# Optimization experiments

Hardware: AMD Instinct MI355X
Metric: run time of the kernel (lower is better)

The kernel has to match this reference:

```python
import jax, jax.numpy as jnp
import numpy as np

H = 768; R = 16; L = 3; NS = 128; NQ = 128


def setup_inputs():
    key = jax.random.key(0)
    ks = iter(jax.random.split(key, 40))
    def w(shape, s=0.02):
        return (s * jax.random.normal(next(ks), shape)).astype(jnp.float32)
    return {
        "support_features": jax.random.normal(next(ks), (NS, H), jnp.float32),
        "support_labels": jax.random.randint(next(ks), (NS,), 0, 3),
        "query_features": jax.random.normal(next(ks), (NQ, H), jnp.float32),
        "sim_w1": w((H, 2 * H)), "sim_b1": jnp.zeros((H,), jnp.float32),
        "sim_w2": w((R, H)), "sim_b2": jnp.zeros((R,), jnp.float32),
        "div_w1": w((H, 2 * H)), "div_b1": jnp.zeros((H,), jnp.float32),
        "div_w2": w((R, H)), "div_b2": jnp.zeros((R,), jnp.float32),
        "rel_w": w((L, R, H, H)), "rel_b": jnp.zeros((L, R, H), jnp.float32),
        "agg_w1": w((L, H, 2 * H)), "agg_b1": jnp.zeros((L, H), jnp.float32),
        "agg_w2": w((L, H, H)), "agg_b2": jnp.zeros((L, H), jnp.float32),
        "ln_g": jnp.ones((L, H), jnp.float32), "ln_b": jnp.zeros((L, H), jnp.float32),
        "cls_w1": w((H // 2, H)), "cls_b1": jnp.zeros((H // 2,), jnp.float32),
        "cls_w2": w((3, H // 2)), "cls_b2": jnp.zeros((3,), jnp.float32),
    }


def _symmetrize(F):
    # torch loop fills [i,j] and [j,i] with value computed from pair (min(i,j), max(i,j)); diag stays 0
    N = F.shape[0]
    idx = jnp.arange(N)
    lower = (idx[:, None] > idx[None, :])
    Fs = jnp.where(lower[:, :, None], jnp.swapaxes(F, 0, 1), F)
    off = (idx[:, None] != idx[None, :]).astype(F.dtype)
    return Fs * off[:, :, None]


def _relations(x, w1, b1, w2, b2, diversity):
    h = x.shape[1]
    wa, wb = w1[:, :h], w1[:, h:]  # split concat([a,b]) @ w1^T into two matmuls
    pa = x @ wa.T                  # [N,H], contribution of first element (x_i)
    if diversity:
        d = jnp.abs(x[:, None, :] - x[None, :, :])   # [N,N,H]
        hid = jax.nn.relu(pa[:, None, :] + d @ wb.T + b1)
    else:
        pb = x @ wb.T
        hid = jax.nn.relu(pa[:, None, :] + pb[None, :, :] + b1)
    logits = hid @ w2.T + b2       # [N,N,R]
    return _symmetrize(jax.nn.softmax(logits, axis=-1))


def _layer_norm(y, g, b):
    mu = y.mean(-1, keepdims=True)
    var = ((y - mu) ** 2).mean(-1, keepdims=True)
    return (y - mu) / jnp.sqrt(var + 1e-5) * g + b


def _prop_layer(x, C, rw, rb, aw1, ab1, aw2, ab2, g, b):
    N = x.shape[0]
    T = jnp.einsum('jh,rkh->jrk', x, rw) + rb       # per-relation transform [N,R,H]
    msg = jnp.einsum('ijr,jrk->ik', C, T) / (N - 1)  # mean over N-1 neighbors (diag of C is 0)
    comb = jnp.concatenate([x, msg], axis=-1)
    agg = jax.nn.relu(comb @ aw1.T + ab1) @ aw2.T + ab2
    return _layer_norm(agg + x, g, b)


def reference(support_features, support_labels, query_features,
              sim_w1, sim_b1, sim_w2, sim_b2,
              div_w1, div_b1, div_w2, div_b2,
              rel_w, rel_b, agg_w1, agg_b1, agg_w2, agg_b2, ln_g, ln_b,
              cls_w1, cls_b1, cls_w2, cls_b2):
    all_x = jnp.concatenate([support_features, query_features], axis=0)
    sim = _relations(all_x, sim_w1, sim_b1, sim_w2, sim_b2, diversity=False)
    div = _relations(all_x, div_w1, div_b1, div_w2, div_b2, diversity=True)
    C = (sim + div) * 0.5
    x = all_x
    for l in range(L):
        x = _prop_layer(x, C, rel_w[l], rel_b[l], agg_w1[l], agg_b1[l],
                        agg_w2[l], agg_b2[l], ln_g[l], ln_b[l])
    q = x[support_features.shape[0]:]
    preds = jax.nn.relu(q @ cls_w1.T + cls_b1) @ cls_w2.T + cls_b2  # dropout = identity (eval)
    return preds, sim, div, x
```

## Files before the change

kernel.cpp:

```cpp
#include <hip/hip_runtime.h>
#include <hip/hip_bf16.h>
#include <hip/hip_fp16.h>


typedef __attribute__((ext_vector_type(8))) short s16x8;
typedef __attribute__((ext_vector_type(4))) float f32x4;

__device__ __forceinline__ short f2bf_s(float f){
  union { __hip_bfloat16 h; short s; } u; u.h = __float2bfloat16(f); return u.s;
}
__device__ __forceinline__ float bf_s2f(short s){
  union { __hip_bfloat16 h; short s; } u; u.s = s; return __bfloat162float(u.h);
}
__device__ __forceinline__ short f2h_s(float f){
  union { __half h; short s; } u; u.h = __float2half(f); return u.s;
}
__device__ __forceinline__ f32x4 mfma16(s16x8 a, s16x8 b, f32x4 c){
  return __builtin_amdgcn_mfma_f32_16x16x32_bf16(a, b, c, 0, 0, 0);
}
__device__ __forceinline__ f32x4 mfma16h(s16x8 a, s16x8 b, f32x4 c){
  return __builtin_amdgcn_mfma_f32_16x16x32_f16(a, b, c, 0, 0, 0);
}
__device__ __forceinline__ void gload16(void* lds, const void* g){
  __builtin_amdgcn_global_load_lds((const __attribute__((address_space(1))) void*)g,
                                   (__attribute__((address_space(3))) void*)lds,
                                   16, 0, 0);
}
__device__ __forceinline__ unsigned pack2bf(float lo, float hi){
  return __builtin_amdgcn_perm(__float_as_uint(hi), __float_as_uint(lo), 0x07060302u);
}
__device__ __forceinline__ s16x8 absdiff_h(uint4 a, uint4 b){
  union { s16x8 v; unsigned u[4]; } o;
  const unsigned au[4] = {a.x,a.y,a.z,a.w}, bu[4] = {b.x,b.y,b.z,b.w};
  #pragma unroll
  for (int w = 0; w < 4; ++w){
    unsigned d;
    asm("v_pk_add_f16 %0, %1, %2 neg_lo:[0,1] neg_hi:[0,1]"
        : "=v"(d) : "v"(au[w]), "v"(bu[w]));
    o.u[w] = d & 0x7fff7fffu;
  }
  return o.v;
}

__device__ __forceinline__ void tri_decode32(int b, int& i0, int& j0){
  int jb = (int)((sqrtf((float)b + 1.f) - 1.f)*0.5f);
  while (4*(jb+1)*(jb+2) <= b) ++jb;
  while (4*jb*(jb+1) > b) --jb;
  i0 = (b - 4*jb*(jb+1))*4;
  j0 = jb*32;
}

template<int BM, int BN, int EPI>
__global__ __launch_bounds__(256) void gemm_bt2(
    const short* __restrict__ A, int lda,
    const short* __restrict__ B, int ldb,
    float* __restrict__ Cf, short* __restrict__ Cb, int ldc,
    const float* __restrict__ bias, int K, int NT)
{
  __shared__ short As[BM*128];
  __shared__ short Bs[BN*128];
  const int tid = threadIdx.x, lane = tid & 63, wid = tid >> 6;
  const int nt = blockIdx.x % NT, mt = blockIdx.x / NT;
  const int m0 = mt*BM, n0 = nt*BN;
  const int wm0 = (wid>>1)*(BM/2), wn0 = (wid&1)*(BN/2);
  f32x4 acc[BM/32][BN/32] = {};
  for (int k0 = 0; k0 < K; k0 += 128){
    if (k0) __syncthreads();
    #pragma unroll
    for (int q = 0; q < BM/16; ++q){
      const int d = (wid*(BM/16)+q)*1024 + lane*16;
      const int row = d>>8, c = d&255;
      gload16((char*)As + (wid*(BM/16)+q)*1024,
              (const char*)A + (size_t)(m0+row)*lda*2 + (size_t)k0*2 + (c ^ ((row&7)<<4)));
    }
    #pragma unroll
    for (int q = 0; q < BN/16; ++q){
      const int d = (wid*(BN/16)+q)*1024 + lane*16;
      const int row = d>>8, c = d&255;
      gload16((char*)Bs + (wid*(BN/16)+q)*1024,
              (const char*)B + (size_t)(n0+row)*ldb*2 + (size_t)k0*2 + (c ^ ((row&7)<<4)));
    }
    __syncthreads();
    #pragma unroll
    for (int kk = 0; kk < 4; ++kk){
      const int colb = (kk*32 + (lane>>4)*8)*2;
      s16x8 af[BM/32], bfv[BN/32];
      #pragma unroll
      for (int mi = 0; mi < BM/32; ++mi){
        const int row = wm0 + mi*16 + (lane&15);
        af[mi] = *(const s16x8*)((char*)As + row*256 + (colb ^ ((row&7)<<4)));
      }
      #pragma unroll
      for (int ni = 0; ni < BN/32; ++ni){
        const int row = wn0 + ni*16 + (lane&15);
        bfv[ni] = *(const s16x8*)((char*)Bs + row*256 + (colb ^ ((row&7)<<4)));
      }
      #pragma unroll
      for (int mi = 0; mi < BM/32; ++mi)
        #pragma unroll
        for (int ni = 0; ni < BN/32; ++ni)
          acc[mi][ni] = mfma16(af[mi], bfv[ni], acc[mi][ni]);
    }
  }
  #pragma unroll
  for (int mi = 0; mi < BM/32; ++mi){
    #pragma unroll
    for (int ni = 0; ni < BN/32; ++ni){
      const int gcol = n0 + wn0 + ni*16 + (lane&15);
      const float bv = bias[gcol];
      #pragma unroll
      for (int r = 0; r < 4; ++r){
        const int grow = m0 + wm0 + mi*16 + (lane>>4)*4 + r;
        float v = acc[mi][ni][r] + bv;
        if (EPI == 2) v = fmaxf(v, 0.f);
        if (EPI == 3) Cf[(size_t)grow*ldc + gcol] = v;
        else          Cb[(size_t)grow*ldc + gcol] = f2bf_s(v);
      }
    }
  }
}

__global__ __launch_bounds__(256) void gemm_msg(
    const short* __restrict__ A,
    const short* __restrict__ B,
    float* __restrict__ slabs)
{
  __shared__ short As[64*64];
  __shared__ short Bs[64*64];
  const int tid = threadIdx.x, lane = tid & 63, wid = tid >> 6;
  const int mt = blockIdx.x / 12, nt = blockIdx.x % 12;
  const int m0 = mt*64, n0 = nt*64, kc0 = blockIdx.y*512;
  const int wm0 = (wid>>1)*32, wn0 = (wid&1)*32;
  f32x4 acc[2][2] = {};
  for (int s = 0; s < 8; ++s){
    const int k0 = kc0 + s*64;
    if (s) __syncthreads();
    #pragma unroll
    for (int q = 0; q < 2; ++q){
      const int d = (wid*2+q)*1024 + lane*16;
      const int row = d>>7, c = d&127;
      gload16((char*)As + (wid*2+q)*1024,
              (const char*)A + (size_t)(m0+row)*8192 + (size_t)k0*2 + (c ^ ((row&7)<<4)));
    }
    #pragma unroll
    for (int rd = 0; rd < 2; ++rd){
      int ei = rd*2048 + tid*8, kr = ei>>6, nc = ei&63;
      union { uint4 v; short s4[8]; } u;
      u.v = *(const uint4*)(B + (size_t)(k0+kr)*768 + n0 + nc);
      #pragma unroll
      for (int e = 0; e < 8; ++e)
        *(short*)((char*)Bs + (nc+e)*128 + ((kr*2) ^ (((nc+e)&7)<<4))) = u.s4[e];
    }
    __syncthreads();
    #pragma unroll
    for (int kk = 0; kk < 2; ++kk){
      const int colb = (kk*32 + (lane>>4)*8)*2;
      s16x8 af[2], bfv[2];
      #pragma unroll
      for (int mi = 0; mi < 2; ++mi){
        const int row = wm0 + mi*16 + (lane&15);
        af[mi] = *(const s16x8*)((char*)As + row*128 + (colb ^ ((row&7)<<4)));
      }
      #pragma unroll
      for (int ni = 0; ni < 2; ++ni){
        const int row = wn0 + ni*16 + (lane&15);
        bfv[ni] = *(const s16x8*)((char*)Bs + row*128 + (colb ^ ((row&7)<<4)));
      }
      #pragma unroll
      for (int mi = 0; mi < 2; ++mi)
        #pragma unroll
        for (int ni = 0; ni < 2; ++ni)
          acc[mi][ni] = mfma16(af[mi], bfv[ni], acc[mi][ni]);
    }
  }
  float* out = slabs + (size_t)blockIdx.y*196608;
  #pragma unroll
  for (int mi = 0; mi < 2; ++mi)
    #pragma unroll
    for (int ni = 0; ni < 2; ++ni){
      const int gcol = n0 + wn0 + ni*16 + (lane&15);
      #pragma unroll
      for (int r = 0; r < 4; ++r){
        const int grow = m0 + wm0 + mi*16 + (lane>>4)*4 + r;
        out[(size_t)grow*768 + gcol] = acc[mi][ni][r];
      }
    }
}

__global__ void msgsum(const float* __restrict__ slabs, short* __restrict__ comb){
  const int i = (blockIdx.x*256 + threadIdx.x)*4;
  if (i >= 196608) return;
  float4 s = {0.f,0.f,0.f,0.f};
  #pragma unroll
  for (int c = 0; c < 8; ++c){
    float4 v = *(const float4*)(slabs + (size_t)c*196608 + i);
    s.x += v.x; s.y += v.y; s.z += v.z; s.w += v.w;
  }
  const float sc = 1.f/255.f;
  const int row = i/768, col = i%768;
  union { uint2 u; short s4[4]; } o;
  o.s4[0]=f2bf_s(s.x*sc); o.s4[1]=f2bf_s(s.y*sc);
  o.s4[2]=f2bf_s(s.z*sc); o.s4[3]=f2bf_s(s.w*sc);
  *(uint2*)(comb + (size_t)row*1536 + 768 + col) = o.u;
}

__global__ __launch_bounds__(512, 4) void pairrel5(
    const short* __restrict__ xh,
    const short* __restrict__ wbdh,
    const float* __restrict__ P2,
    const short* __restrict__ w2d_g,
    const short* __restrict__ w2s_g,
    float* __restrict__ Ldp,
    float* __restrict__ Ls)
{
  __shared__ short Bs[2*256*64];
  const int tid = threadIdx.x, lane = tid & 63, wv = tid >> 6;
  int i0, j0; tri_decode32(blockIdx.x, i0, j0);

  if (blockIdx.y == 3){
    f32x4 acc2 = {0.f,0.f,0.f,0.f};
    const int arow = wv*16 + (lane&15);
    for (int nt = 0; nt < 3; ++nt){
      const int n0 = nt*256;
      if (nt) __syncthreads();
      {
        const int row = tid>>2, c0 = (tid&3)*64;
        const float* pap = P2 + (size_t)(i0 + (row>>5))*2304 + n0 + c0;
        const float* pbp = P2 + (size_t)(j0 + (row&31))*2304 + 768 + n0 + c0;
        #pragma unroll
        for (int cc = 0; cc < 64; cc += 8){
          float4 a0 = *(const float4*)(pap+cc), a1 = *(const float4*)(pap+cc+4);
          float4 q0 = *(const float4*)(pbp+cc), q1 = *(const float4*)(pbp+cc+4);
          uint4 o;
          o.x = pack2bf(fmaxf(a0.x+q0.x,0.f), fmaxf(a0.y+q0.y,0.f));
          o.y = pack2bf(fmaxf(a0.z+q0.z,0.f), fmaxf(a0.w+q0.w,0.f));
          o.z = pack2bf(fmaxf(a1.x+q1.x,0.f), fmaxf(a1.y+q1.y,0.f));
          o.w = pack2bf(fmaxf(a1.z+q1.z,0.f), fmaxf(a1.w+q1.w,0.f));
          *(uint4*)((char*)Bs + row*512 + (((c0+cc)*2) ^ ((row&7)<<4))) = o;
        }
      }
      __syncthreads();
      #pragma unroll
      for (int q = 0; q < 8; ++q){
        const int colb = (q*32 + (lane>>4)*8)*2;
        s16x8 a = *(const s16x8*)((const char*)Bs + arow*512 + (colb ^ ((arow&7)<<4)));
        s16x8 w = *(const s16x8*)(w2s_g + (size_t)(lane&15)*768 + n0 + q*32 + (lane>>4)*8);
        acc2 = mfma16(a, w, acc2);
      }
    }
    const int r_ = lane & 15;
    #pragma unroll
    for (int r = 0; r < 4; ++r){
      const int p = wv*16 + (lane>>4)*4 + r;
      const int i = i0 + (p>>5), j = j0 + (p&31);
      Ls[(((size_t)i<<8) + j)*16 + r_] = acc2[r];
    }
    return;
  }

  const int ip = wv >> 2, jj = (wv >> 1) & 1, wc = wv & 1;
  const int nt = blockIdx.y, n0 = nt*256;

  const short* xjp  = xh + (size_t)(j0 + jj*16 + (lane&15))*768 + (lane>>4)*8;
  const short* xi0p = xh + (size_t)(i0 + 2*ip    )*768 + (lane>>4)*8;
  const short* xi1p = xh + (size_t)(i0 + 2*ip + 1)*768 + (lane>>4)*8;

  #pragma unroll
  for (int q = 0; q < 4; ++q){
    const int d = (wv*4+q)*1024 + lane*16;
    const int row = d>>7, c = d&127;
    gload16((char*)Bs + (wv*4+q)*1024,
            (const char*)wbdh + (size_t)(n0+row)*1536 + (c ^ ((row&7)<<4)));
  }

  f32x4 acc[2][8] = {};
  for (int t = 0; t < 12; ++t){
    uint4 uja  = *(const uint4*)(xjp  + t*64);
    uint4 ujb  = *(const uint4*)(xjp  + t*64 + 32);
    uint4 ui0a = *(const uint4*)(xi0p + t*64);
    uint4 ui0b = *(const uint4*)(xi0p + t*64 + 32);
    uint4 ui1a = *(const uint4*)(xi1p + t*64);
    uint4 ui1b = *(const uint4*)(xi1p + t*64 + 32);
    if (t < 11){
      char* dst = (char*)Bs + ((t+1)&1)*32768;
      const char* src = (const char*)wbdh + (size_t)(t+1)*128;
      #pragma unroll
      for (int q = 0; q < 4; ++q){
        const int d = (wv*4+q)*1024 + lane*16;
        const int row = d>>7, c = d&127;
        gload16(dst + (wv*4+q)*1024, src + (size_t)(n0+row)*1536 + (c ^ ((row&7)<<4)));
      }
    }
    __builtin_amdgcn_sched_barrier(0);
    if (t < 11) asm volatile("s_waitcnt vmcnt(10)" ::: "memory");
    else        asm volatile("s_waitcnt vmcnt(6)"  ::: "memory");
    __builtin_amdgcn_s_barrier();
    __builtin_amdgcn_sched_barrier(0);
    const char* bufc = (const char*)Bs + (t&1)*32768;
    #pragma unroll
    for (int kk = 0; kk < 2; ++kk){
      s16x8 af0 = absdiff_h(kk ? ujb : uja, kk ? ui0b : ui0a);
      s16x8 af1 = absdiff_h(kk ? ujb : uja, kk ? ui1b : ui1a);
      const int colb = (kk*32 + (lane>>4)*8)*2;
      #pragma unroll
      for (int ni = 0; ni < 8; ++ni){
        const int row = wc*128 + ni*16 + (lane&15);
        s16x8 bv = *(const s16x8*)(bufc + row*128 + (colb ^ ((row&7)<<4)));
        acc[0][ni] = mfma16h(af0, bv, acc[0][ni]);
        acc[1][ni] = mfma16h(af1, bv, acc[1][ni]);
      }
    }
    __builtin_amdgcn_sched_barrier(0);
    __builtin_amdgcn_s_barrier();
  }
  __syncthreads();

  float* red = (float*)((char*)Bs + 32768);
  #pragma unroll
  for (int h = 0; h < 2; ++h){
    if (ip == h){
      #pragma unroll
      for (int mi = 0; mi < 2; ++mi){
        const float* pr = P2 + (size_t)(i0 + 2*h + mi)*2304 + 1536 + n0;
        #pragma unroll
        for (int ni = 0; ni < 8; ++ni){
          const int col = wc*128 + ni*16 + (lane&15);
          const float pav = pr[col];
          #pragma unroll
          for (int r = 0; r < 4; ++r){
            const int lrow = mi*32 + jj*16 + (lane>>4)*4 + r;
            const float v = fmaxf(acc[mi][ni][r] + pav, 0.f);
            *(short*)((char*)Bs + lrow*512 + ((col*2) ^ ((lrow&7)<<4))) =
                (short)(__float_as_uint(v) >> 16);
          }
        }
      }
    }
    __syncthreads();
    const int kh = wv >> 2, rq = wv & 3;
    f32x4 a2 = {0.f,0.f,0.f,0.f};
    const int arow = rq*16 + (lane&15);
    #pragma unroll
    for (int q = 0; q < 4; ++q){
      const int k = kh*128 + q*32 + (lane>>4)*8;
      s16x8 a = *(const s16x8*)((char*)Bs + arow*512 + ((k*2) ^ ((arow&7)<<4)));
      s16x8 w = *(const s16x8*)(w2d_g + (size_t)(lane&15)*768 + n0 + k);
      a2 = mfma16(a, w, a2);
    }
    if (kh == 1){
      #pragma unroll
      for (int r = 0; r < 4; ++r)
        red[(rq*16 + (lane>>4)*4 + r)*16 + (lane&15)] = a2[r];
    }
    __syncthreads();
    if (kh == 0){
      #pragma unroll
      for (int r = 0; r < 4; ++r){
        const int lrow = rq*16 + (lane>>4)*4 + r;
        const int p = h*64 + lrow;
        const int i = i0 + (p>>5), j = j0 + (p&31);
        Ldp[(size_t)nt*1048576 + (((size_t)i<<8) + j)*16 + (lane&15)]
          = a2[r] + red[lrow*16 + (lane&15)];
      }
    }
    __syncthreads();
  }
}

__global__ __launch_bounds__(256) void finisher2(
    const float* __restrict__ Ls, const float* __restrict__ Ldp,
    const float* __restrict__ b2s, const float* __restrict__ b2d,
    float* __restrict__ simo, float* __restrict__ divo, short* __restrict__ Cb)
{
  const int p = blockIdx.x*256 + threadIdx.x;
  const int i = p >> 8, j = p & 255;
  float so[16], dd[16];
  if (i == j){
    #pragma unroll
    for (int r = 0; r < 16; ++r){ so[r] = 0.f; dd[r] = 0.f; }
  } else {
    const int si = i < j ? i : j, sj = i < j ? j : i;
    const size_t base = (((size_t)si << 8) + sj) * 16;
    float mx = -1e30f, sum;
    #pragma unroll
    for (int r = 0; r < 16; ++r){ so[r] = Ls[base+r] + b2s[r]; mx = fmaxf(mx, so[r]); }
    sum = 0.f;
    #pragma unroll
    for (int r = 0; r < 16; ++r){ so[r] = expf(so[r]-mx); sum += so[r]; }
    sum = 1.f/sum;
    #pragma unroll
    for (int r = 0; r < 16; ++r) so[r] *= sum;
    mx = -1e30f;
    #pragma unroll
    for (int r = 0; r < 16; ++r){
      dd[r] = Ldp[base+r] + Ldp[base+r+1048576] + Ldp[base+r+2097152] + b2d[r];
      mx = fmaxf(mx, dd[r]);
    }
    sum = 0.f;
    #pragma unroll
    for (int r = 0; r < 16; ++r){ dd[r] = expf(dd[r]-mx); sum += dd[r]; }
    sum = 1.f/sum;
    #pragma unroll
    for (int r = 0; r < 16; ++r) dd[r] *= sum;
  }
  const size_t ob = (size_t)p * 16;
  #pragma unroll
  for (int r = 0; r < 16; ++r){
    simo[ob+r] = so[r];
    divo[ob+r] = dd[r];
    Cb[ob+r]   = f2bf_s(0.5f*(so[r]+dd[r]));
  }
}

__global__ __launch_bounds__(256) void gemm_relT(
    const short* __restrict__ A,
    const float* __restrict__ Bf,
    short* __restrict__ T,
    const float* __restrict__ bias)
{
  __shared__ short As[128*64];
  __shared__ short Bs[64*64];
  const int tid = threadIdx.x, lane = tid & 63, wv = tid >> 6;
  const int nt = blockIdx.x >> 1, mt = blockIdx.x & 1;
  const int n0 = nt*64, m0 = mt*128;
  const int wm = wv >> 1, wn = wv & 1;
  const int brow = tid >> 2, q4 = tid & 3;
  f32x4 acc[4][2] = {};
  for (int k0 = 0; k0 < 768; k0 += 64){
    if (k0) __syncthreads();
    #pragma unroll
    for (int q = 0; q < 4; ++q){
      const int d = (wv*4+q)*1024 + lane*16;
      const int row = d>>7, c = d&127;
      gload16((char*)As + (wv*4+q)*1024,
              (const char*)A + (size_t)(m0+row)*3072 + (size_t)k0*2 + (c ^ ((row&7)<<4)));
    }
    {
      const float* bp = Bf + (size_t)(n0+brow)*768 + k0 + q4*16;
      float4 v0 = *(const float4*)bp,      v1 = *(const float4*)(bp+4);
      float4 v2 = *(const float4*)(bp+8),  v3 = *(const float4*)(bp+12);
      union { uint4 v; unsigned u[4]; } ua, ub;
      ua.u[0]=pack2bf(v0.x,v0.y); ua.u[1]=pack2bf(v0.z,v0.w);
      ua.u[2]=pack2bf(v1.x,v1.y); ua.u[3]=pack2bf(v1.z,v1.w);
      ub.u[0]=pack2bf(v2.x,v2.y); ub.u[1]=pack2bf(v2.z,v2.w);
      ub.u[2]=pack2bf(v3.x,v3.y); ub.u[3]=pack2bf(v3.z,v3.w);
      const int bc = q4*32;
      *(uint4*)((char*)Bs + brow*128 + ((bc   ) ^ ((brow&7)<<4))) = ua.v;
      *(uint4*)((char*)Bs + brow*128 + ((bc+16) ^ ((brow&7)<<4))) = ub.v;
    }
    __syncthreads();
    #pragma unroll
    for (int kk = 0; kk < 2; ++kk){
      const int kb = kk*64 + (lane>>4)*16;
      s16x8 af[4], bfv[2];
      #pragma unroll
      for (int mi = 0; mi < 4; ++mi){
        const int row = wm*64 + mi*16 + (lane&15);
        af[mi] = *(const s16x8*)((char*)As + row*128 + (kb ^ ((row&7)<<4)));
      }
      #pragma unroll
      for (int ni = 0; ni < 2; ++ni){
        const int row = wn*32 + ni*16 + (lane&15);
        bfv[ni] = *(const s16x8*)((char*)Bs + row*128 + (kb ^ ((row&7)<<4)));
      }
      #pragma unroll
      for (int mi = 0; mi < 4; ++mi)
        #pragma unroll
        for (int ni = 0; ni < 2; ++ni)
          acc[mi][ni] = mfma16(af[mi], bfv[ni], acc[mi][ni]);
    }
  }
  #pragma unroll
  for (int mi = 0; mi < 4; ++mi)
    #pragma unroll
    for (int ni = 0; ni < 2; ++ni){
      const int nn = n0 + wn*32 + ni*16 + (lane&15);
      const float bv = bias[nn];
      #pragma unroll
      for (int r = 0; r < 4; ++r){
        const int row = m0 + wm*64 + mi*16 + (lane>>4)*4 + r;
        T[(size_t)row*12288 + nn] = f2bf_s(acc[mi][ni][r] + bv);
      }
    }
}

__global__ __launch_bounds__(256) void ln_kernel(
    const float* __restrict__ y, float* __restrict__ x, short* __restrict__ combx,
    const float* __restrict__ g, const float* __restrict__ b, float* __restrict__ xfinal)
{
  const int row = blockIdx.x, tid = threadIdx.x;
  float tv[3]; float s = 0.f, s2 = 0.f;
  #pragma unroll
  for (int c = 0; c < 3; ++c){
    const int idx = tid + c*256;
    const float v = y[row*768+idx] + x[row*768+idx];
    tv[c] = v; s += v; s2 += v*v;
  }
  #pragma unroll
  for (int off = 32; off > 0; off >>= 1){ s += __shfl_down(s, off); s2 += __shfl_down(s2, off); }
  __shared__ float red[8];
  const int wid = tid >> 6, lane = tid & 63;
  if (lane == 0){ red[wid] = s; red[wid+4] = s2; }
  __syncthreads();
  if (tid == 0){
    red[0] = red[0]+red[1]+red[2]+red[3];
    red[4] = red[4]+red[5]+red[6]+red[7];
  }
  __syncthreads();
  const float mu = red[0]*(1.f/768.f);
  const float var = red[4]*(1.f/768.f) - mu*mu;
  const float inv = rsqrtf(var + 1e-5f);
  #pragma unroll
  for (int c = 0; c < 3; ++c){
    const int idx = tid + c*256;
    const float v = (tv[c]-mu)*inv*g[idx] + b[idx];
    x[row*768+idx] = v;
    combx[(size_t)row*1536 + idx] = f2bf_s(v);
    if (xfinal) xfinal[row*768+idx] = v;
  }
}

__device__ __forceinline__ void cvt4(const float* __restrict__ s,
                                     short* __restrict__ d, int i, int n){
  if (i >= n) return;
  float4 v = *(const float4*)(s+i);
  union { uint2 u; short s4[4]; } o;
  o.s4[0]=f2bf_s(v.x); o.s4[1]=f2bf_s(v.y); o.s4[2]=f2bf_s(v.z); o.s4[3]=f2bf_s(v.w);
  *(uint2*)(d+i) = o.u;
}

__global__ void setup_all(
    const float* __restrict__ sim_w2, const float* __restrict__ div_w2,
    const float* __restrict__ agg_w1, const float* __restrict__ agg_w2,
    const float* __restrict__ cls_w1, const float* __restrict__ sim_w1,
    const float* __restrict__ div_w1, const float* __restrict__ sup,
    const float* __restrict__ qry, const float* __restrict__ sim_b1,
    const float* __restrict__ div_b1,
    short* __restrict__ W2S, short* __restrict__ W2D, short* __restrict__ AW1,
    short* __restrict__ AW2, short* __restrict__ CW1, short* __restrict__ W1X4,
    float* __restrict__ XF, short* __restrict__ COMB, float* __restrict__ B1C,
    short* __restrict__ XH, short* __restrict__ WBDH)
{
  const int b = blockIdx.x, tid = threadIdx.x;
  if (b < 12)        cvt4(sim_w2, W2S, (b*256+tid)*4, 12288);
  else if (b < 24)   cvt4(div_w2, W2D, ((b-12)*256+tid)*4, 12288);
  else if (b < 3480) cvt4(agg_w1, AW1, ((b-24)*256+tid)*4, 3538944);
  else if (b < 5208) cvt4(agg_w2, AW2, ((b-3480)*256+tid)*4, 1769472);
  else if (b < 5496) cvt4(cls_w1, CW1, ((b-5208)*256+tid)*4, 294912);
  else if (b < 7800){
    const int i = ((b-5496)*256+tid)*4;
    if (i < 2359296){
      const int mat = i / 589824, rem = i % 589824;
      const int r = rem / 768, c = rem % 768;
      const float* src = (mat < 2 ? sim_w1 : div_w1) + (size_t)r*1536 + (mat&1)*768 + c;
      float4 v = *(const float4*)src;
      union { uint2 u; short s4[4]; } o;
      o.s4[0]=f2bf_s(v.x); o.s4[1]=f2bf_s(v.y); o.s4[2]=f2bf_s(v.z); o.s4[3]=f2bf_s(v.w);
      *(uint2*)(W1X4+i) = o.u;
    }
  } else if (b < 7992){
    const int i = ((b-7800)*256+tid)*4;
    if (i < 196608){
      const int row = i / 768, col = i % 768;
      const float* s = (row < 128 ? sup + (size_t)row*768 : qry + (size_t)(row-128)*768) + col;
      float4 v = *(const float4*)s;
      *(float4*)(XF+i) = v;
      union { uint2 u; short s4[4]; } o;
      o.s4[0]=f2bf_s(v.x); o.s4[1]=f2bf_s(v.y); o.s4[2]=f2bf_s(v.z); o.s4[3]=f2bf_s(v.w);
      *(uint2*)(COMB + (size_t)row*1536 + col) = o.u;
      union { uint2 u; short s4[4]; } oh;
      oh.s4[0]=f2h_s(v.x); oh.s4[1]=f2h_s(v.y); oh.s4[2]=f2h_s(v.z); oh.s4[3]=f2h_s(v.w);
      *(uint2*)(XH + i) = oh.u;
    }
  } else if (b < 7993){
    for (int t = tid; t < 2304; t += 256)
      B1C[t] = (t < 768) ? sim_b1[t] : ((t < 1536) ? 0.f : div_b1[t-1536]);
  } else {
    const int i = ((b-7993)*256+tid)*4;
    if (i < 589824){
      const int r = i / 768, c = i % 768;
      float4 v = *(const float4*)(div_w1 + (size_t)r*1536 + 768 + c);
      union { uint2 u; short s4[4]; } o;
      o.s4[0]=f2h_s(v.x); o.s4[1]=f2h_s(v.y); o.s4[2]=f2h_s(v.z); o.s4[3]=f2h_s(v.w);
      *(uint2*)(WBDH + i) = o.u;
    }
  }
}

__global__ void cls2_kernel(const short* __restrict__ hc, const float* __restrict__ w2,
                            const float* __restrict__ b2, float* __restrict__ preds){
  const int t = blockIdx.x*192 + threadIdx.x;
  if (t >= 384) return;
  const int m = t/3, c = t - m*3;
  float s = b2[c];
  for (int k = 0; k < 384; ++k)
    s += bf_s2f(hc[m*384+k]) * w2[c*384+k];
  preds[m*3+c] = s;
}

static const size_t OFF_B1CAT = 0;
static const size_t OFF_LS    = 16384;
static const size_t OFF_MSGF  = 4210688;
static const size_t OFF_LDP   = 10502144;
static const size_t OFF_P     = 23085056;
static const size_t OFF_XF    = 25444352;
static const size_t OFF_Y     = 26230784;
static const size_t OFF_COMB  = 27017216;
static const size_t OFF_CB    = 27803648;
static const size_t OFF_W1X4  = 29900800;
static const size_t OFF_W2S   = 34619392;
static const size_t OFF_W2D   = 34643968;
static const size_t OFF_AW1   = 34668544;
static const size_t OFF_AW2   = 41746432;
static const size_t OFF_CW1   = 45285376;
static const size_t OFF_TBUF  = 45875200;
static const size_t OFF_HID1  = 52166656;
static const size_t OFF_HIDC  = 52559872;
static const size_t OFF_XH    = 52658176;
static const size_t OFF_WBDH  = 53051392;

extern "C" void kernel_launch(void* const* d_in, const int* in_sizes, int n_in,
                              void* d_out, int out_size, void* d_ws, size_t ws_size,
                              hipStream_t stream)
{
  (void)in_sizes; (void)n_in; (void)out_size; (void)ws_size;
  const float* sup    = (const float*)d_in[0];
  const float* qry    = (const float*)d_in[2];
  const float* sim_w1 = (const float*)d_in[3];
  const float* sim_b1 = (const float*)d_in[4];
  const float* sim_w2 = (const float*)d_in[5];
  const float* sim_b2 = (const float*)d_in[6];
  const float* div_w1 = (const float*)d_in[7];
  const float* div_b1 = (const float*)d_in[8];
  const float* div_w2 = (const float*)d_in[9];
  const float* div_b2 = (const float*)d_in[10];
  const float* rel_w  = (const float*)d_in[11];
  const float* rel_b  = (const float*)d_in[12];
  const float* agg_w1 = (const float*)d_in[13];
  const float* agg_b1 = (const float*)d_in[14];
  const float* agg_w2 = (const float*)d_in[15];
  const float* agg_b2 = (const float*)d_in[16];
  const float* ln_g   = (const float*)d_in[17];
  const float* ln_b   = (const float*)d_in[18];
  const float* cls_w1 = (const float*)d_in[19];
  const float* cls_b1 = (const float*)d_in[20];
  const float* cls_w2 = (const float*)d_in[21];
  const float* cls_b2 = (const float*)d_in[22];

  char* w = (char*)d_ws;
  float* B1C  = (float*)(w + OFF_B1CAT);
  float* LS   = (float*)(w + OFF_LS);
  float* MSGF = (float*)(w + OFF_MSGF);
  float* LDP  = (float*)(w + OFF_LDP);
  float* P2   = (float*)(w + OFF_P);
  float* XF   = (float*)(w + OFF_XF);
  float* Y    = (float*)(w + OFF_Y);
  short* COMB = (short*)(w + OFF_COMB);
  short* CB   = (short*)(w + OFF_CB);
  short* W1X4 = (short*)(w + OFF_W1X4);
  short* W2S  = (short*)(w + OFF_W2S);
  short* W2D  = (short*)(w + OFF_W2D);
  short* AW1  = (short*)(w + OFF_AW1);
  short* AW2  = (short*)(w + OFF_AW2);
  short* CW1  = (short*)(w + OFF_CW1);
  short* TBUF = (short*)(w + OFF_TBUF);
  short* HID1 = (short*)(w + OFF_HID1);
  short* HIDC = (short*)(w + OFF_HIDC);
  short* XH   = (short*)(w + OFF_XH);
  short* WBDH = (short*)(w + OFF_WBDH);

  float* preds = (float*)d_out;
  float* simo  = preds + 384;
  float* divo  = simo + 1048576;
  float* xout  = divo + 1048576;

  setup_all<<<8569, 256, 0, stream>>>(sim_w2, div_w2, agg_w1, agg_w2, cls_w1,
                                      sim_w1, div_w1, sup, qry, sim_b1, div_b1,
                                      W2S, W2D, AW1, AW2, CW1, W1X4, XF, COMB, B1C,
                                      XH, WBDH);

  gemm_bt2<64,64,3><<<144, 256, 0, stream>>>(COMB, 1536, W1X4, 768, P2, nullptr, 2304,
                                             B1C, 768, 36);

  pairrel5<<<dim3(288,4), 512, 0, stream>>>(XH, WBDH, P2, W2D, W2S, LDP, LS);
  finisher2<<<256, 256, 0, stream>>>(LS, LDP, sim_b2, div_b2, simo, divo, CB);

  for (int l = 0; l < 3; ++l){
    gemm_relT<<<384, 256, 0, stream>>>(COMB, rel_w + (size_t)l*9437184, TBUF,
                                       rel_b + l*12288);
    gemm_msg<<<dim3(48,8), 256, 0, stream>>>(CB, TBUF, MSGF);
    msgsum<<<192, 256, 0, stream>>>(MSGF, COMB);
    gemm_bt2<32,32,2><<<192, 256, 0, stream>>>(COMB, 1536, AW1 + (size_t)l*1179648, 1536,
                                               nullptr, HID1, 768, agg_b1 + l*768, 1536, 24);
    gemm_bt2<32,32,3><<<192, 256, 0, stream>>>(HID1, 768, AW2 + (size_t)l*589824, 768,
                                               Y, nullptr, 768, agg_b2 + l*768, 768, 24);
    ln_kernel<<<256, 256, 0, stream>>>(Y, XF, COMB, ln_g + l*768, ln_b + l*768,
                                       (l == 2) ? xout : nullptr);
  }

  gemm_bt2<32,32,2><<<48, 256, 0, stream>>>(COMB + (size_t)128*1536, 1536, CW1, 768,
                                            nullptr, HIDC, 384, cls_b1, 768, 12);
  cls2_kernel<<<2, 192, 0, stream>>>(HIDC, cls_w2, cls_b2, preds);
}
```

Measured before the change: 321.2 us.

## Enlarge diversity pair tile to 8x32 and split similarity path into separate kernel

The pairwise diversity kernel now handles 8 i-rows per block instead of 4, so each block loads a weight tile once and reuses it across twice as many rows. That halves the block count and roughly doubles accumulator registers, so launch bounds drop to 2 blocks per SM. The similarity-logit branch, which previously ran as an extra blockIdx.y slice of the same kernel, moves into its own smaller kernel over 4x16 triangular tiles. The cost is higher register pressure and lower occupancy in the main kernel, plus one extra launch.

```diff
diff --git a/kernel.cpp b/kernel.cpp
--- a/kernel.cpp
+++ b/kernel.cpp
@@ -42,11 +42,18 @@
   return o.v;
 }
 
-__device__ __forceinline__ void tri_decode32(int b, int& i0, int& j0){
-  int jb = (int)((sqrtf((float)b + 1.f) - 1.f)*0.5f);
-  while (4*(jb+1)*(jb+2) <= b) ++jb;
-  while (4*jb*(jb+1) > b) --jb;
-  i0 = (b - 4*jb*(jb+1))*4;
+__device__ __forceinline__ void tri_decode(int b, int& i0, int& j0){
+  int jb = (int)((sqrtf(2.f*(float)b + 1.f) - 1.f)*0.5f);
+  while (2*(jb+1)*(jb+2) <= b) ++jb;
+  while (2*jb*(jb+1) > b) --jb;
+  i0 = (b - 2*jb*(jb+1))*4;
+  j0 = jb*16;
+}
+__device__ __forceinline__ void tri_decode8x32(int b, int& i0, int& j0){
+  int jb = (int)((sqrtf(2.f*(float)b + 1.f) - 1.f)*0.5f);
+  while (2*(jb+1)*(jb+2) <= b) ++jb;
+  while (2*jb*(jb+1) > b) --jb;
+  i0 = (b - 2*jb*(jb+1))*8;
   j0 = jb*32;
 }
 
@@ -204,66 +211,21 @@
   *(uint2*)(comb + (size_t)row*1536 + 768 + col) = o.u;
 }
 
-__global__ __launch_bounds__(512, 4) void pairrel5(
+__global__ __launch_bounds__(512, 2) void pairrel7(
     const short* __restrict__ xh,
     const short* __restrict__ wbdh,
     const float* __restrict__ P2,
     const short* __restrict__ w2d_g,
-    const short* __restrict__ w2s_g,
-    float* __restrict__ Ldp,
-    float* __restrict__ Ls)
+    float* __restrict__ Ldp)
 {
   __shared__ short Bs[2*256*64];
   const int tid = threadIdx.x, lane = tid & 63, wv = tid >> 6;
-  int i0, j0; tri_decode32(blockIdx.x, i0, j0);
-
-  if (blockIdx.y == 3){
-    f32x4 acc2 = {0.f,0.f,0.f,0.f};
-    const int arow = wv*16 + (lane&15);
-    for (int nt = 0; nt < 3; ++nt){
-      const int n0 = nt*256;
-      if (nt) __syncthreads();
-      {
-        const int row = tid>>2, c0 = (tid&3)*64;
-        const float* pap = P2 + (size_t)(i0 + (row>>5))*2304 + n0 + c0;
-        const float* pbp = P2 + (size_t)(j0 + (row&31))*2304 + 768 + n0 + c0;
-        #pragma unroll
-        for (int cc = 0; cc < 64; cc += 8){
-          float4 a0 = *(const float4*)(pap+cc), a1 = *(const float4*)(pap+cc+4);
-          float4 q0 = *(const float4*)(pbp+cc), q1 = *(const float4*)(pbp+cc+4);
-          uint4 o;
-          o.x = pack2bf(fmaxf(a0.x+q0.x,0.f), fmaxf(a0.y+q0.y,0.f));
-          o.y = pack2bf(fmaxf(a0.z+q0.z,0.f), fmaxf(a0.w+q0.w,0.f));
-          o.z = pack2bf(fmaxf(a1.x+q1.x,0.f), fmaxf(a1.y+q1.y,0.f));
-          o.w = pack2bf(fmaxf(a1.z+q1.z,0.f), fmaxf(a1.w+q1.w,0.f));
-          *(uint4*)((char*)Bs + row*512 + (((c0+cc)*2) ^ ((row&7)<<4))) = o;
-        }
-      }
-      __syncthreads();
-      #pragma unroll
-      for (int q = 0; q < 8; ++q){
-        const int colb = (q*32 + (lane>>4)*8)*2;
-        s16x8 a = *(const s16x8*)((const char*)Bs + arow*512 + (colb ^ ((arow&7)<<4)));
-        s16x8 w = *(const s16x8*)(w2s_g + (size_t)(lane&15)*768 + n0 + q*32 + (lane>>4)*8);
-        acc2 = mfma16(a, w, acc2);
-      }
-    }
-    const int r_ = lane & 15;
-    #pragma unroll
-    for (int r = 0; r < 4; ++r){
-      const int p = wv*16 + (lane>>4)*4 + r;
-      const int i = i0 + (p>>5), j = j0 + (p&31);
-      Ls[(((size_t)i<<8) + j)*16 + r_] = acc2[r];
-    }
-    return;
-  }
-
   const int ip = wv >> 2, jj = (wv >> 1) & 1, wc = wv & 1;
+  int i0, j0; tri_decode8x32(blockIdx.x, i0, j0);
   const int nt = blockIdx.y, n0 = nt*256;
 
-  const short* xjp  = xh + (size_t)(j0 + jj*16 + (lane&15))*768 + (lane>>4)*8;
-  const short* xi0p = xh + (size_t)(i0 + 2*ip    )*768 + (lane>>4)*8;
-  const short* xi1p = xh + (size_t)(i0 + 2*ip + 1)*768 + (lane>>4)*8;
+  const short* xjp = xh + (size_t)(j0 + jj*16 + (lane&15))*768 + (lane>>4)*8;
+  const short* xib = xh + (size_t)(i0 + 4*ip)*768 + (lane>>4)*8;
 
   #pragma unroll
   for (int q = 0; q < 4; ++q){
@@ -273,14 +235,16 @@
             (const char*)wbdh + (size_t)(n0+row)*1536 + (c ^ ((row&7)<<4)));
   }
 
-  f32x4 acc[2][8] = {};
+  f32x4 acc[4][8] = {};
   for (int t = 0; t < 12; ++t){
-    uint4 uja  = *(const uint4*)(xjp  + t*64);
-    uint4 ujb  = *(const uint4*)(xjp  + t*64 + 32);
-    uint4 ui0a = *(const uint4*)(xi0p + t*64);
-    uint4 ui0b = *(const uint4*)(xi0p + t*64 + 32);
-    uint4 ui1a = *(const uint4*)(xi1p + t*64);
-    uint4 ui1b = *(const uint4*)(xi1p + t*64 + 32);
+    uint4 uja = *(const uint4*)(xjp + t*64);
+    uint4 ujb = *(const uint4*)(xjp + t*64 + 32);
+    uint4 uia[4], uib[4];
+    #pragma unroll
+    for (int mi = 0; mi < 4; ++mi){
+      uia[mi] = *(const uint4*)(xib + (size_t)mi*768 + t*64);
+      uib[mi] = *(const uint4*)(xib + (size_t)mi*768 + t*64 + 32);
+    }
     if (t < 11){
       char* dst = (char*)Bs + ((t+1)&1)*32768;
       const char* src = (const char*)wbdh + (size_t)(t+1)*128;
@@ -292,22 +256,25 @@
       }
     }
     __builtin_amdgcn_sched_barrier(0);
-    if (t < 11) asm volatile("s_waitcnt vmcnt(10)" ::: "memory");
-    else        asm volatile("s_waitcnt vmcnt(6)"  ::: "memory");
+    if (t < 11) asm volatile("s_waitcnt vmcnt(14)" ::: "memory");
+    else        asm volatile("s_waitcnt vmcnt(10)" ::: "memory");
     __builtin_amdgcn_s_barrier();
     __builtin_amdgcn_sched_barrier(0);
     const char* bufc = (const char*)Bs + (t&1)*32768;
     #pragma unroll
     for (int kk = 0; kk < 2; ++kk){
-      s16x8 af0 = absdiff_h(kk ? ujb : uja, kk ? ui0b : ui0a);
-      s16x8 af1 = absdiff_h(kk ? ujb : uja, kk ? ui1b : ui1a);
+      s16x8 af[4];
+      #pragma unroll
+      for (int mi = 0; mi < 4; ++mi)
+        af[mi] = absdiff_h(kk ? ujb : uja, kk ? uib[mi] : uia[mi]);
       const int colb = (kk*32 + (lane>>4)*8)*2;
       #pragma unroll
       for (int ni = 0; ni < 8; ++ni){
         const int row = wc*128 + ni*16 + (lane&15);
         s16x8 bv = *(const s16x8*)(bufc + row*128 + (colb ^ ((row&7)<<4)));
-        acc[0][ni] = mfma16h(af0, bv, acc[0][ni]);
-        acc[1][ni] = mfma16h(af1, bv, acc[1][ni]);
+        #pragma unroll
+        for (int mi = 0; mi < 4; ++mi)
+          acc[mi][ni] = mfma16h(af[mi], bv, acc[mi][ni]);
       }
     }
     __builtin_amdgcn_sched_barrier(0);
@@ -316,19 +283,21 @@
   __syncthreads();
 
   float* red = (float*)((char*)Bs + 32768);
-  #pragma unroll
-  for (int h = 0; h < 2; ++h){
-    if (ip == h){
-      #pragma unroll
-      for (int mi = 0; mi < 2; ++mi){
-        const float* pr = P2 + (size_t)(i0 + 2*h + mi)*2304 + 1536 + n0;
+  const int kh = wv >> 2, rq = wv & 3;
+  #pragma unroll
+  for (int h = 0; h < 4; ++h){
+    if (ip == (h>>1)){
+      #pragma unroll
+      for (int q = 0; q < 2; ++q){
+        const int mi = 2*(h&1) + q;
+        const float* pr = P2 + (size_t)(i0 + 4*ip + mi)*2304 + 1536 + n0;
         #pragma unroll
         for (int ni = 0; ni < 8; ++ni){
           const int col = wc*128 + ni*16 + (lane&15);
           const float pav = pr[col];
           #pragma unroll
           for (int r = 0; r < 4; ++r){
-            const int lrow = mi*32 + jj*16 + (lane>>4)*4 + r;
+            const int lrow = q*32 + jj*16 + (lane>>4)*4 + r;
             const float v = fmaxf(acc[mi][ni][r] + pav, 0.f);
             *(short*)((char*)Bs + lrow*512 + ((col*2) ^ ((lrow&7)<<4))) =
                 (short)(__float_as_uint(v) >> 16);
@@ -337,12 +306,11 @@
       }
     }
     __syncthreads();
-    const int kh = wv >> 2, rq = wv & 3;
     f32x4 a2 = {0.f,0.f,0.f,0.f};
     const int arow = rq*16 + (lane&15);
     #pragma unroll
-    for (int q = 0; q < 4; ++q){
-      const int k = kh*128 + q*32 + (lane>>4)*8;
+    for (int qq = 0; qq < 4; ++qq){
+      const int k = kh*128 + qq*32 + (lane>>4)*8;
       s16x8 a = *(const s16x8*)((char*)Bs + arow*512 + ((k*2) ^ ((arow&7)<<4)));
       s16x8 w = *(const s16x8*)(w2d_g + (size_t)(lane&15)*768 + n0 + k);
       a2 = mfma16(a, w, a2);
@@ -364,6 +332,53 @@
       }
     }
     __syncthreads();
+  }
+}
+
+__global__ __launch_bounds__(256) void simpart(
+    const float* __restrict__ P2,
+    const short* __restrict__ w2s_g,
+    float* __restrict__ Ls)
+{
+  __shared__ short Hs[64*256];
+  const int tid = threadIdx.x, lane = tid & 63, wv = tid >> 6;
+  int i0, j0; tri_decode(blockIdx.x, i0, j0);
+  const int arow = wv*16 + (lane&15);
+  f32x4 acc2 = {0.f,0.f,0.f,0.f};
+  for (int nt = 0; nt < 3; ++nt){
+    const int n0 = nt*256;
+    if (nt) __syncthreads();
+    {
+      const int row = tid>>2, c0 = (tid&3)*64;
+      const float* pap = P2 + (size_t)(i0 + (row>>4))*2304 + n0 + c0;
+      const float* pbp = P2 + (size_t)(j0 + (row&15))*2304 + 768 + n0 + c0;
+      #pragma unroll
+      for (int cc = 0; cc < 64; cc += 8){
+        float4 a0 = *(const float4*)(pap+cc), a1 = *(const float4*)(pap+cc+4);
+        float4 q0 = *(const float4*)(pbp+cc), q1 = *(const float4*)(pbp+cc+4);
+        uint4 o;
+        o.x = pack2bf(fmaxf(a0.x+q0.x,0.f), fmaxf(a0.y+q0.y,0.f));
+        o.y = pack2bf(fmaxf(a0.z+q0.z,0.f), fmaxf(a0.w+q0.w,0.f));
+        o.z = pack2bf(fmaxf(a1.x+q1.x,0.f), fmaxf(a1.y+q1.y,0.f));
+        o.w = pack2bf(fmaxf(a1.z+q1.z,0.f), fmaxf(a1.w+q1.w,0.f));
+        *(uint4*)((char*)Hs + row*512 + (((c0+cc)*2) ^ ((row&7)<<4))) = o;
+      }
+    }
+    __syncthreads();
+    #pragma unroll
+    for (int q = 0; q < 8; ++q){
+      const int colb = (q*32 + (lane>>4)*8)*2;
+      s16x8 a = *(const s16x8*)((const char*)Hs + arow*512 + (colb ^ ((arow&7)<<4)));
+      s16x8 w = *(const s16x8*)(w2s_g + (size_t)(lane&15)*768 + n0 + q*32 + (lane>>4)*8);
+      acc2 = mfma16(a, w, acc2);
+    }
+  }
+  const int r_ = lane & 15;
+  #pragma unroll
+  for (int r = 0; r < 4; ++r){
+    const int p = wv*16 + (lane>>4)*4 + r;
+    const int i = i0 + (p>>4), j = j0 + (p&15);
+    Ls[(((size_t)i<<8) + j)*16 + r_] = acc2[r];
   }
 }
 
@@ -682,7 +697,8 @@
   gemm_bt2<64,64,3><<<144, 256, 0, stream>>>(COMB, 1536, W1X4, 768, P2, nullptr, 2304,
                                              B1C, 768, 36);
 
-  pairrel5<<<dim3(288,4), 512, 0, stream>>>(XH, WBDH, P2, W2D, W2S, LDP, LS);
+  pairrel7<<<dim3(144,3), 512, 0, stream>>>(XH, WBDH, P2, W2D, LDP);
+  simpart<<<544, 256, 0, stream>>>(P2, W2S, LS);
   finisher2<<<256, 256, 0, stream>>>(LS, LDP, sim_b2, div_b2, simo, divo, CB);
 
   for (int l = 0; l < 3; ++l){
```

Result: faster. 307.8 us (-4.1%).
